# Performance work log

Measured on AMD Instinct MI355X. Metric: run time of the kernel, lower is better.

The kernel has to match this reference:

```python
import jax, jax.numpy as jnp
import numpy as np

N, E = 50000, 500000
A, R, EB, EH, H, C, AH, SH, S, AV = 64, 20, 32, 64, 4, 32, 128, 64, 32, 32
EPS = 1e-8
MAX_DIST = 0.5   # nm, maximum_interaction_radius
SCALE = 1.0      # nm, scale_factor


def physnet_rbf(d):
    # PhysNet radial basis: exp(-beta * (exp(-d) - mu_k)^2), mu_k in [exp(-r_cut), 1]
    mu = jnp.linspace(np.exp(-MAX_DIST), 1.0, R).astype(jnp.float32)
    beta = jnp.float32((2.0 / R * (1.0 - np.exp(-MAX_DIST))) ** -2)
    return jnp.exp(-beta * (jnp.exp(-d)[:, None] - mu) ** 2)  # [E, R]


def _forward(h, x, v, idx_i, idx_j, W_edge_in, b_edge_in, W_edge_h, b_edge_h,
             W_edge_out, b_edge_out, W_att, b_att, W_x_mix, W_node1, b_node1,
             W_node2, b_node2, W_post1, b_post1, W_post2, b_post2,
             W_vel1, b_vel1, W_vel2, w_v_mix):
    n = h.shape[0]
    act = jax.nn.silu
    seg_sum = lambda t, idx: jax.ops.segment_sum(t, idx, num_segments=n)

    # geometry
    r_ij = x[idx_j] - x[idx_i]                       # [E,3]
    d_ij = jnp.sqrt(jnp.sum(r_ij * r_ij, -1) + EPS)  # [E]
    dir_ij = r_ij / (d_ij[:, None] + EPS)            # [E,3]

    # update_edge: gather, RBF filter, edge MLP
    h_cat = jnp.concatenate([h[idx_i], h[idx_j]], -1)                 # [E,2A]
    filtered = physnet_rbf(d_ij) * (h_cat @ W_edge_in + b_edge_in)    # [E,R]
    e_in = jnp.concatenate([h_cat, filtered, d_ij[:, None] / SCALE], -1)
    h_ij_edge = act(e_in @ W_edge_h + b_edge_h) @ W_edge_out + b_edge_out  # [E,EB]

    # semantic attention: CELU logits + segment softmax over receivers per head
    logits = jax.nn.celu(h_ij_edge @ W_att + b_att, alpha=2.0)        # [E,H]
    seg_max = jax.ops.segment_max(logits, idx_i, num_segments=n)      # [n,H]
    exp_l = jnp.exp(logits - seg_max[idx_i])
    denom = seg_sum(exp_l, idx_i)
    att = exp_l / (denom[idx_i] + EPS)                                # [E,H]
    h_ij_semantic = (att[:, :, None] * h_ij_edge[:, None, :]).reshape(-1, H * EB)

    # neighborhood aggregation (scatter-add)
    h_i_semantic = seg_sum(h_ij_semantic, idx_i)                      # [n,H*EB]

    # spatial attention
    mix = jnp.tanh(h_ij_semantic @ W_x_mix)                           # [E,C]
    combinations = dir_ij[:, None, :] * mix[:, :, None]               # [E,C,3]
    counts = jnp.maximum(seg_sum(jnp.ones((idx_i.shape[0],), h.dtype), idx_i), 1.0)
    comb_mean = seg_sum(combinations, idx_i) / counts[:, None, None]  # scatter-mean
    comb_norm2 = jnp.sum(comb_mean * comb_mean, -1)                   # [n,C]
    h_i_spatial = act(act(comb_norm2 @ W_post1 + b_post1) @ W_post2 + b_post2)

    # node update (residual)
    node_in = jnp.concatenate([h, h_i_semantic, h_i_spatial], -1)
    h_upd = h + act(act(node_in @ W_node1 + b_node1) @ W_node2 + b_node2)

    # velocity / coordinate update
    v_ij = jnp.einsum('ecx,c->ex', combinations, w_v_mix)             # [E,3]
    dv = seg_sum(v_ij, idx_i) / counts[:, None]                       # scatter-mean
    gate = 2.0 * jax.nn.sigmoid(act(h_upd @ W_vel1 + b_vel1) @ W_vel2)  # [n,1]
    v_upd = gate * v + dv
    x_upd = x + v_upd
    return h_upd, x_upd, v_upd


def _p(k, shape, scale=0.05):
    return jax.random.normal(k, shape, dtype=jnp.float32) * scale


def setup_inputs() -> dict:
    key = jax.random.key(0)
    ks = jax.random.split(key, 24)
    return {
        'h': jax.random.normal(ks[0], (N, A), dtype=jnp.float32),
        'x': jax.random.normal(ks[1], (N, 3), dtype=jnp.float32),
        'v': jax.random.normal(ks[2], (N, 3), dtype=jnp.float32),
        'idx_i': jax.random.randint(ks[3], (E,), 0, N),
        'idx_j': jax.random.randint(ks[4], (E,), 0, N),
        'W_edge_in': _p(ks[5], (2 * A, R)), 'b_edge_in': jnp.zeros((R,), jnp.float32),
        'W_edge_h': _p(ks[6], (2 * A + R + 1, EH)), 'b_edge_h': jnp.zeros((EH,), jnp.float32),
        'W_edge_out': _p(ks[7], (EH, EB)), 'b_edge_out': jnp.zeros((EB,), jnp.float32),
        'W_att': _p(ks[8], (EB, H)), 'b_att': jnp.zeros((H,), jnp.float32),
        'W_x_mix': _p(ks[9], (H * EB, C)),
        'W_node1': _p(ks[10], (A + H * EB + S, AH)), 'b_node1': jnp.zeros((AH,), jnp.float32),
        'W_node2': _p(ks[11], (AH, A)), 'b_node2': jnp.zeros((A,), jnp.float32),
        'W_post1': _p(ks[12], (C, SH)), 'b_post1': jnp.zeros((SH,), jnp.float32),
        'W_post2': _p(ks[13], (SH, S)), 'b_post2': jnp.zeros((S,), jnp.float32),
        'W_vel1': _p(ks[14], (A, AV)), 'b_vel1': jnp.zeros((AV,), jnp.float32),
        'W_vel2': _p(ks[15], (AV, 1)),
        'w_v_mix': _p(ks[16], (C,)),
    }


def reference(h, x, v, idx_i, idx_j, W_edge_in, b_edge_in, W_edge_h, b_edge_h,
              W_edge_out, b_edge_out, W_att, b_att, W_x_mix, W_node1, b_node1,
              W_node2, b_node2, W_post1, b_post1, W_post2, b_post2,
              W_vel1, b_vel1, W_vel2, w_v_mix):
    return _forward(h, x, v, idx_i, idx_j, W_edge_in, b_edge_in, W_edge_h, b_edge_h,
                    W_edge_out, b_edge_out, W_att, b_att, W_x_mix, W_node1, b_node1,
                    W_node2, b_node2, W_post1, b_post1, W_post2, b_post2,
                    W_vel1, b_vel1, W_vel2, w_v_mix)
```

## Files before the change

kernel.cpp:

```cpp
#include <hip/hip_runtime.h>
#include <math.h>

#define DA 64
#define NODEIN_DIM 224
#define EPSC 1e-8f

typedef short v8s __attribute__((ext_vector_type(8)));
typedef float v4f __attribute__((ext_vector_type(4)));
typedef unsigned short ushort_t;

__device__ __forceinline__ float siluf(float v) {
  return v * __builtin_amdgcn_rcpf(1.0f + __expf(-v));
}
__device__ __forceinline__ float tanhfast(float x) {
  return 1.0f - 2.0f * __builtin_amdgcn_rcpf(__expf(2.0f * x) + 1.0f);
}

__device__ __forceinline__ void atomAddF(float* p, float v) {
#if defined(__HIP_DEVICE_COMPILE__)
  unsafeAtomicAdd(p, v);
#else
  atomicAdd(p, v);
#endif
}

__device__ __forceinline__ unsigned short f2bfu(float f) {
  union { float f; unsigned u; } v; v.f = f;
  unsigned r = v.u + 0x7fffu + ((v.u >> 16) & 1u);
  return (unsigned short)(r >> 16);
}
__device__ __forceinline__ short f2bfs(float f) { return (short)f2bfu(f); }
__device__ __forceinline__ float bf2f(ushort_t s) {
  union { unsigned u; float f; } v; v.u = ((unsigned)s) << 16; return v.f;
}

#define MU0 0.60653065971263342f
#define DMU ((1.0f - 0.60653065971263342f) / 19.0f)
#define BETA ((float)(1.0 / (0.039346934028736658 * 0.039346934028736658)))

__global__ __launch_bounds__(256) void cast_count(
    const float* __restrict__ hsrc, ushort_t* __restrict__ hb, int n4,
    const int* __restrict__ idx_i, int* __restrict__ deg, int E)
{
  const int stride = gridDim.x * blockDim.x;
  for (int i = blockIdx.x * blockDim.x + threadIdx.x; i < n4; i += stride) {
    const float4 fv = ((const float4*)hsrc)[i];
    ushort4 o;
    o.x = f2bfu(fv.x); o.y = f2bfu(fv.y); o.z = f2bfu(fv.z); o.w = f2bfu(fv.w);
    ((ushort4*)hb)[i] = o;
  }
  for (int e = blockIdx.x * blockDim.x + threadIdx.x; e < E; e += stride)
    atomicAdd(&deg[idx_i[e]], 1);
}

#define SCAN_B 64
#define SCAN_T (SCAN_B * 256)

__global__ __launch_bounds__(256) void deg_tsum(
    const int* __restrict__ deg, int* __restrict__ tsum, int N, int C)
{
  const int g = blockIdx.x * blockDim.x + threadIdx.x;
  const int lo = g * C;
  const int hi = (lo + C < N) ? (lo + C) : N;
  int s = 0;
  for (int i = lo; i < hi; ++i) s += deg[i];
  tsum[g] = s;
}

__global__ __launch_bounds__(256) void scan_tsum(int* __restrict__ tsum)
{
  __shared__ int ps[256];
  const int t = threadIdx.x;
  const int per = SCAN_T / 256;
  const int lo = t * per;
  int s = 0;
  for (int i = 0; i < per; ++i) s += tsum[lo + i];
  ps[t] = s;
  __syncthreads();
  if (t == 0) {
    int a = 0;
    for (int i = 0; i < 256; ++i) { const int v = ps[i]; ps[i] = a; a += v; }
  }
  __syncthreads();
  int acc = ps[t];
  for (int i = 0; i < per; ++i) {
    const int v = tsum[lo + i];
    tsum[lo + i] = acc;
    acc += v;
  }
}

__global__ __launch_bounds__(256) void write_csr(
    const int* __restrict__ deg, const int* __restrict__ tpre,
    int* __restrict__ rowstart, int* __restrict__ cursor, int N, int C)
{
  const int g = blockIdx.x * blockDim.x + threadIdx.x;
  const int lo = g * C;
  const int hi = (lo + C < N) ? (lo + C) : N;
  int acc = tpre[g];
  for (int i = lo; i < hi; ++i) {
    const int d = deg[i];
    rowstart[i] = acc;
    cursor[i] = acc;
    acc += d;
  }
  if (hi == N) rowstart[N] = acc;
}

__global__ __launch_bounds__(256) void bucket_edges(
    const int* __restrict__ idx_i, const int* __restrict__ idx_j,
    int* __restrict__ cursor, int2* __restrict__ ijperm, int E)
{
  const int stride = gridDim.x * blockDim.x;
  for (int e = blockIdx.x * blockDim.x + threadIdx.x; e < E; e += stride) {
    const int ii = idx_i[e];
    const int pos = atomicAdd(&cursor[ii], 1);
    ijperm[pos] = make_int2(ii, idx_j[e]);
  }
}

#define THS 72
__global__ __launch_bounds__(256) void edge_f12(
    const ushort_t* __restrict__ h_bf, const float* __restrict__ x,
    const int2* __restrict__ ijperm,
    const float* __restrict__ W_in, const float* __restrict__ b_in,
    const float* __restrict__ W_h, const float* __restrict__ b_h,
    const float* __restrict__ W_out, const float* __restrict__ b_out,
    const float* __restrict__ W_att, const float* __restrict__ b_att,
    float4* __restrict__ dirb, ushort_t* __restrict__ heb,
    float* __restrict__ expl, float* __restrict__ denom, int E)
{
  __shared__ ushort_t sB1[8 * 512];
  __shared__ ushort_t sB2[20 * 512];
  __shared__ ushort_t tH[4][16 * THS];

  const int tid = threadIdx.x;
  for (int idx = tid; idx < 8 * 512; idx += 256) {
    const int j = idx & 7;
    const int ln = (idx >> 3) & 63;
    const int f = idx >> 9;
    const int k = (f >> 1) * 32 + (ln >> 4) * 8 + j;
    const int col = (f & 1) * 16 + (ln & 15);
    sB1[idx] = (col < 20) ? f2bfu(W_in[k * 20 + col]) : (ushort_t)0;
  }
  for (int idx = tid; idx < 20 * 512; idx += 256) {
    const int j = idx & 7;
    const int ln = (idx >> 3) & 63;
    const int f = idx >> 9;
    const int k = (f >> 2) * 32 + (ln >> 4) * 8 + j;
    const int col = (f & 3) * 16 + (ln & 15);
    sB2[idx] = (k < 149) ? f2bfu(W_h[k * 64 + col]) : (ushort_t)0;
  }
  __syncthreads();

  const int gtid = blockIdx.x * blockDim.x + tid;
  const int wid = gtid >> 6;
  const int lane = tid & 63;
  const int w = tid >> 6;
  const int nw = (gridDim.x * blockDim.x) >> 6;
  const int l15 = lane & 15;
  const int q = lane >> 4;

  const ushort_t* b1l = sB1 + lane * 8;
  const ushort_t* b2l = sB2 + lane * 8;

  v8s bfr3[2][2];
  #pragma unroll
  for (int kc = 0; kc < 2; ++kc)
    #pragma unroll
    for (int nt = 0; nt < 2; ++nt)
      #pragma unroll
      for (int j = 0; j < 8; ++j) {
        const int k = kc * 32 + q * 8 + j;
        const int col = nt * 16 + l15;
        bfr3[kc][nt][j] = f2bfs(W_out[k * 32 + col]);
      }

  float bin[2], mu[2];
  #pragma unroll
  for (int nt = 0; nt < 2; ++nt) {
    const int col = nt * 16 + l15;
    bin[nt] = (col < 20) ? b_in[col] : 0.0f;
    mu[nt] = MU0 + (float)col * DMU;
  }
  float bias2[4];
  #pragma unroll
  for (int nt = 0; nt < 4; ++nt) bias2[nt] = b_h[nt * 16 + l15];
  float bias3[2];
  #pragma unroll
  for (int nt = 0; nt < 2; ++nt) bias3[nt] = b_out[nt * 16 + l15];

  v8s battf;
  #pragma unroll
  for (int j = 0; j < 8; ++j)
    battf[j] = (l15 < 4) ? f2bfs(W_att[(q * 8 + j) * 4 + l15]) : (short)0;
  const float bav = (l15 < 4) ? b_att[l15] : 0.0f;

  const int ntiles = (E + 15) >> 4;

  int iiC = 0, jjC = 0;
  v8s afr[4];
  float rCx = 0.f, rCy = 0.f, rCz = 0.f;
  if (wid < ntiles) {
    const int row0 = wid * 16 + l15;
    const int rowL0 = (row0 < E) ? row0 : (E - 1);
    const int2 ij = ijperm[rowL0];
    iiC = ij.x;
    jjC = ij.y;
    afr[0] = *(const v8s*)(h_bf + (size_t)iiC * 64 + q * 8);
    afr[1] = *(const v8s*)(h_bf + (size_t)iiC * 64 + 32 + q * 8);
    afr[2] = *(const v8s*)(h_bf + (size_t)jjC * 64 + q * 8);
    afr[3] = *(const v8s*)(h_bf + (size_t)jjC * 64 + 32 + q * 8);
    if (lane < 16) {
      rCx = x[jjC * 3 + 0] - x[iiC * 3 + 0];
      rCy = x[jjC * 3 + 1] - x[iiC * 3 + 1];
      rCz = x[jjC * 3 + 2] - x[iiC * 3 + 2];
    }
  }

  for (int t = wid; t < ntiles; t += nw) {
    const int tn = t + nw;
    int iiN = 0, jjN = 0;
    v8s nfr[4];
    float rNx = 0.f, rNy = 0.f, rNz = 0.f;
    if (tn < ntiles) {
      const int rowN = tn * 16 + l15;
      const int rowLN = (rowN < E) ? rowN : (E - 1);
      const int2 ij = ijperm[rowLN];
      iiN = ij.x;
      jjN = ij.y;
      nfr[0] = *(const v8s*)(h_bf + (size_t)iiN * 64 + q * 8);
      nfr[1] = *(const v8s*)(h_bf + (size_t)iiN * 64 + 32 + q * 8);
      nfr[2] = *(const v8s*)(h_bf + (size_t)jjN * 64 + q * 8);
      nfr[3] = *(const v8s*)(h_bf + (size_t)jjN * 64 + 32 + q * 8);
      if (lane < 16) {
        rNx = x[jjN * 3 + 0] - x[iiN * 3 + 0];
        rNy = x[jjN * 3 + 1] - x[iiN * 3 + 1];
        rNz = x[jjN * 3 + 2] - x[iiN * 3 + 2];
      }
    }

    const int row = t * 16 + l15;
    float dval = 0.0f;
    if (lane < 16) {
      const float s2 = rCx * rCx + rCy * rCy + rCz * rCz + EPSC;
      const float rv = __builtin_amdgcn_rsqf(s2);
      dval = s2 * rv;
      if (row < E) {
        float4 dq;
        dq.x = rCx * rv; dq.y = rCy * rv; dq.z = rCz * rv; dq.w = dval;
        dirb[row] = dq;
      }
    }

    v4f acc1[2];
    #pragma unroll
    for (int nt = 0; nt < 2; ++nt) {
      v4f a = {0.f, 0.f, 0.f, 0.f};
      #pragma unroll
      for (int kc = 0; kc < 4; ++kc) {
        const v8s bfrag = *(const v8s*)(b1l + (kc * 2 + nt) * 512);
        a = __builtin_amdgcn_mfma_f32_16x16x32_bf16(afr[kc], bfrag, a, 0, 0, 0);
      }
      acc1[nt] = a;
    }

    float dr[4], edr[4];
    #pragma unroll
    for (int r = 0; r < 4; ++r) {
      dr[r] = __shfl(dval, q * 4 + r);
      edr[r] = __expf(-dr[r]);
    }
    #pragma unroll
    for (int nt = 0; nt < 2; ++nt) {
      const int col = nt * 16 + l15;
      #pragma unroll
      for (int r = 0; r < 4; ++r) {
        ushort_t ov;
        if (col < 20) {
          const float tt = edr[r] - mu[nt];
          ov = f2bfu((acc1[nt][r] + bin[nt]) * __expf(-BETA * tt * tt));
        } else if (col == 20) {
          ov = f2bfu(dr[r]);
        } else {
          ov = 0;
        }
        tH[w][(q * 4 + r) * THS + col] = ov;
      }
    }
    __builtin_amdgcn_wave_barrier();

    const v8s afr4 = *(const v8s*)&tH[w][l15 * THS + q * 8];
    __builtin_amdgcn_wave_barrier();

    v4f acc2[4];
    #pragma unroll
    for (int nt = 0; nt < 4; ++nt) {
      v4f a = {0.f, 0.f, 0.f, 0.f};
      #pragma unroll
      for (int kc = 0; kc < 4; ++kc) {
        const v8s bfrag = *(const v8s*)(b2l + (kc * 4 + nt) * 512);
        a = __builtin_amdgcn_mfma_f32_16x16x32_bf16(afr[kc], bfrag, a, 0, 0, 0);
      }
      const v8s bfrag4 = *(const v8s*)(b2l + (4 * 4 + nt) * 512);
      a = __builtin_amdgcn_mfma_f32_16x16x32_bf16(afr4, bfrag4, a, 0, 0, 0);
      acc2[nt] = a;
    }

    #pragma unroll
    for (int nt = 0; nt < 4; ++nt) {
      #pragma unroll
      for (int r = 0; r < 4; ++r)
        tH[w][(q * 4 + r) * THS + nt * 16 + l15] =
            f2bfu(siluf(acc2[nt][r] + bias2[nt]));
    }
    __builtin_amdgcn_wave_barrier();

    v8s af3[2];
    af3[0] = *(const v8s*)&tH[w][l15 * THS + q * 8];
    af3[1] = *(const v8s*)&tH[w][l15 * THS + 32 + q * 8];

    v4f acc3[2];
    #pragma unroll
    for (int nt = 0; nt < 2; ++nt) {
      v4f a = {0.f, 0.f, 0.f, 0.f};
      #pragma unroll
      for (int kc = 0; kc < 2; ++kc)
        a = __builtin_amdgcn_mfma_f32_16x16x32_bf16(af3[kc], bfr3[kc][nt], a, 0, 0, 0);
      acc3[nt] = a;
    }
    __builtin_amdgcn_wave_barrier();

    const int rowb = t * 16 + q * 4;
    #pragma unroll
    for (int nt = 0; nt < 2; ++nt) {
      const int col = nt * 16 + l15;
      #pragma unroll
      for (int r = 0; r < 4; ++r) {
        const ushort_t hv = f2bfu(acc3[nt][r] + bias3[nt]);
        tH[w][(q * 4 + r) * THS + col] = hv;
        if (rowb + r < E) heb[(size_t)(rowb + r) * 32 + col] = hv;
      }
    }
    __builtin_amdgcn_wave_barrier();

    const v8s afA = *(const v8s*)&tH[w][l15 * THS + q * 8];
    v4f az = {0.f, 0.f, 0.f, 0.f};
    const v4f aacc = __builtin_amdgcn_mfma_f32_16x16x32_bf16(afA, battf, az, 0, 0, 0);

    int ii_r[4];
    #pragma unroll
    for (int r = 0; r < 4; ++r) ii_r[r] = __shfl(iiC, q * 4 + r);

    if (l15 < 4) {
      #pragma unroll
      for (int r = 0; r < 4; ++r) {
        if (rowb + r < E) {
          const float la = aacc[r] + bav;
          const float l = (la > 0.f) ? la : 2.0f * (__expf(0.5f * la) - 1.0f);
          const float ev = __expf(l);
          expl[(size_t)(rowb + r) * 4 + l15] = ev;
          atomAddF(&denom[ii_r[r] * 4 + l15], ev);
        }
      }
    }
    __builtin_amdgcn_wave_barrier();

    iiC = iiN; jjC = jjN;
    afr[0] = nfr[0]; afr[1] = nfr[1]; afr[2] = nfr[2]; afr[3] = nfr[3];
    rCx = rNx; rCy = rNy; rCz = rNz;
  }
}

__global__ __launch_bounds__(256) void node_fused(
    const int* __restrict__ rowstart,
    const ushort_t* __restrict__ heb,
    const float* __restrict__ expl, const float* __restrict__ denom,
    const float4* __restrict__ dirb,
    const float* __restrict__ W_xmix, const float* __restrict__ w_vmix,
    ushort_t* __restrict__ hsem, float* __restrict__ norm2,
    float* __restrict__ dv_mean, int N)
{
  __shared__ ushort_t sBX[8 * 512];

  const int tid = threadIdx.x;
  for (int idx = tid; idx < 8 * 512; idx += 256) {
    const int j = idx & 7;
    const int ln = (idx >> 3) & 63;
    const int f = idx >> 9;
    const int k = (f >> 1) * 32 + (ln >> 4) * 8 + j;
    const int col = (f & 1) * 16 + (ln & 15);
    sBX[idx] = f2bfu(W_xmix[k * 32 + col]);
  }
  __syncthreads();

  const int gtid = blockIdx.x * blockDim.x + tid;
  const int wid = gtid >> 6;
  const int lane = tid & 63;
  const int nw = (gridDim.x * blockDim.x) >> 6;
  const int l15 = lane & 15;
  const int q = lane >> 4;
  const ushort_t* bXl = sBX + lane * 8;

  const float wv0 = w_vmix[l15];
  const float wv1 = w_vmix[16 + l15];

  int sC = 0, eC = 0;
  if (wid < N) {
    sC = rowstart[wid];
    eC = rowstart[wid + 1];
  }

  for (int n = wid; n < N; n += nw) {
    const int nn = n + nw;
    int sN = 0, eN = 0;
    if (nn < N) {
      sN = rowstart[nn];
      eN = rowstart[nn + 1];
    }
    const int s = sC;
    const int epd = eC;
    const int deg = epd - s;

    v8s hech0 = {0, 0, 0, 0, 0, 0, 0, 0};
    if (deg > 0) {
      const int e0 = s + ((l15 < deg) ? l15 : (deg - 1));
      hech0 = *(const v8s*)(heb + e0 * 32 + q * 8);
    }

    const float4 dnm = *(const float4*)(denom + n * 4);
    float invden[4];
    invden[0] = __builtin_amdgcn_rcpf(dnm.x + EPSC);
    invden[1] = __builtin_amdgcn_rcpf(dnm.y + EPSC);
    invden[2] = __builtin_amdgcn_rcpf(dnm.z + EPSC);
    invden[3] = __builtin_amdgcn_rcpf(dnm.w + EPSC);

    {
      float sm00 = 0.f, sm01 = 0.f, sm10 = 0.f, sm11 = 0.f;
      float sm20 = 0.f, sm21 = 0.f, sm30 = 0.f, sm31 = 0.f;
      int k = s;
      for (; k + 4 <= epd; k += 4) {
        const unsigned hv = ((const unsigned*)heb)[k * 16 + lane];
        const float4 ex = ((const float4*)expl)[k + q];
        const float h0 = bf2f((ushort_t)(hv & 0xffffu));
        const float h1 = bf2f((ushort_t)(hv >> 16));
        sm00 += ex.x * h0; sm01 += ex.x * h1;
        sm10 += ex.y * h0; sm11 += ex.y * h1;
        sm20 += ex.z * h0; sm21 += ex.z * h1;
        sm30 += ex.w * h0; sm31 += ex.w * h1;
      }
      if (k < epd) {
        const int ke = k + q;
        const int kl = (ke < epd) ? ke : (epd - 1);
        const float live = (ke < epd) ? 1.0f : 0.0f;
        const unsigned hv = ((const unsigned*)heb)[kl * 16 + l15];
        const float4 ex = ((const float4*)expl)[kl];
        const float h0 = bf2f((ushort_t)(hv & 0xffffu)) * live;
        const float h1 = bf2f((ushort_t)(hv >> 16)) * live;
        sm00 += ex.x * h0; sm01 += ex.x * h1;
        sm10 += ex.y * h0; sm11 += ex.y * h1;
        sm20 += ex.z * h0; sm21 += ex.z * h1;
        sm30 += ex.w * h0; sm31 += ex.w * h1;
      }
      sm00 += __shfl_xor(sm00, 16); sm00 += __shfl_xor(sm00, 32);
      sm01 += __shfl_xor(sm01, 16); sm01 += __shfl_xor(sm01, 32);
      sm10 += __shfl_xor(sm10, 16); sm10 += __shfl_xor(sm10, 32);
      sm11 += __shfl_xor(sm11, 16); sm11 += __shfl_xor(sm11, 32);
      sm20 += __shfl_xor(sm20, 16); sm20 += __shfl_xor(sm20, 32);
      sm21 += __shfl_xor(sm21, 16); sm21 += __shfl_xor(sm21, 32);
      sm30 += __shfl_xor(sm30, 16); sm30 += __shfl_xor(sm30, 32);
      sm31 += __shfl_xor(sm31, 16); sm31 += __shfl_xor(sm31, 32);
      const float sa = (q & 2) ? ((q & 1) ? sm30 : sm20)
                               : ((q & 1) ? sm10 : sm00);
      const float sb = (q & 2) ? ((q & 1) ? sm31 : sm21)
                               : ((q & 1) ? sm11 : sm01);
      const float idn = (q & 2) ? ((q & 1) ? invden[3] : invden[2])
                                : ((q & 1) ? invden[1] : invden[0]);
      const unsigned pack = (unsigned)f2bfu(sa * idn) |
                            ((unsigned)f2bfu(sb * idn) << 16);
      ((unsigned*)hsem)[n * 64 + lane] = pack;
    }

    float cx0 = 0.f, cy0 = 0.f, cz0 = 0.f;
    float cx1 = 0.f, cy1 = 0.f, cz1 = 0.f;

    for (int c0 = 0; c0 < deg; c0 += 16) {
      v8s hech;
      if (c0 == 0) {
        hech = hech0;
      } else {
        const int ra = c0 + l15;
        const int eA = s + ((ra < deg) ? ra : (deg - 1));
        hech = *(const v8s*)(heb + eA * 32 + q * 8);
      }

      v4f y[4][2];
      #pragma unroll
      for (int h4 = 0; h4 < 4; ++h4) {
        #pragma unroll
        for (int nt = 0; nt < 2; ++nt) {
          v4f z = {0.f, 0.f, 0.f, 0.f};
          y[h4][nt] = __builtin_amdgcn_mfma_f32_16x16x32_bf16(
              hech, *(const v8s*)(bXl + (h4 * 2 + nt) * 512), z, 0, 0, 0);
        }
      }

      #pragma unroll
      for (int r = 0; r < 4; ++r) {
        const int rr = c0 + q * 4 + r;
        const int live = rr < deg;
        const int eR = s + (live ? rr : (deg - 1));
        const float lf = live ? 1.0f : 0.0f;
        const float4 ex4 = *(const float4*)(expl + eR * 4);
        const float at0 = ex4.x * invden[0] * lf;
        const float at1 = ex4.y * invden[1] * lf;
        const float at2 = ex4.z * invden[2] * lf;
        const float at3 = ex4.w * invden[3] * lf;
        const float p0 = at0 * y[0][0][r] + at1 * y[1][0][r] +
                         at2 * y[2][0][r] + at3 * y[3][0][r];
        const float p1 = at0 * y[0][1][r] + at1 * y[1][1][r] +
                         at2 * y[2][1][r] + at3 * y[3][1][r];
        const float4 dq = dirb[eR];
        const float m0 = tanhfast(p0);
        const float m1 = tanhfast(p1);
        cx0 += dq.x * m0; cy0 += dq.y * m0; cz0 += dq.z * m0;
        cx1 += dq.x * m1; cy1 += dq.y * m1; cz1 += dq.z * m1;
      }
    }

    cx0 += __shfl_xor(cx0, 16); cx0 += __shfl_xor(cx0, 32);
    cy0 += __shfl_xor(cy0, 16); cy0 += __shfl_xor(cy0, 32);
    cz0 += __shfl_xor(cz0, 16); cz0 += __shfl_xor(cz0, 32);
    cx1 += __shfl_xor(cx1, 16); cx1 += __shfl_xor(cx1, 32);
    cy1 += __shfl_xor(cy1, 16); cy1 += __shfl_xor(cy1, 32);
    cz1 += __shfl_xor(cz1, 16); cz1 += __shfl_xor(cz1, 32);

    const float cinv = __builtin_amdgcn_rcpf(fmaxf((float)deg, 1.0f));

    if (lane < 32) {
      const float mx = ((lane & 16) ? cx1 : cx0) * cinv;
      const float my = ((lane & 16) ? cy1 : cy0) * cinv;
      const float mz = ((lane & 16) ? cz1 : cz0) * cinv;
      norm2[n * 32 + lane] = mx * mx + my * my + mz * mz;
    }

    float tx = wv0 * cx0 + wv1 * cx1;
    float ty = wv0 * cy0 + wv1 * cy1;
    float tz = wv0 * cz0 + wv1 * cz1;
    tx += __shfl_xor(tx, 1); tx += __shfl_xor(tx, 2);
    tx += __shfl_xor(tx, 4); tx += __shfl_xor(tx, 8);
    ty += __shfl_xor(ty, 1); ty += __shfl_xor(ty, 2);
    ty += __shfl_xor(ty, 4); ty += __shfl_xor(ty, 8);
    tz += __shfl_xor(tz, 1); tz += __shfl_xor(tz, 2);
    tz += __shfl_xor(tz, 4); tz += __shfl_xor(tz, 8);
    if (lane == 0) {
      dv_mean[n * 3 + 0] = tx * cinv;
      dv_mean[n * 3 + 1] = ty * cinv;
      dv_mean[n * 3 + 2] = tz * cinv;
    }

    sC = sN; eC = eN;
  }
}

#define W1S 232
__global__ __launch_bounds__(256) void node_c1_mfma(
    const ushort_t* __restrict__ h_bf, const ushort_t* __restrict__ hsem,
    const float* __restrict__ norm2,
    const float* __restrict__ W_post1, const float* __restrict__ b_post1,
    const float* __restrict__ W_post2, const float* __restrict__ b_post2,
    const float* __restrict__ W_node1, const float* __restrict__ b_node1,
    ushort_t* __restrict__ nh_out, int N)
{
  __shared__ ushort_t sW1t[128 * W1S];
  __shared__ ushort_t tp[4][16 * THS];

  const int tid = threadIdx.x;
  for (int idx = tid; idx < 224 * 128; idx += 256) {
    const int k = idx >> 7;
    const int c = idx & 127;
    sW1t[c * W1S + k] = f2bfu(W_node1[idx]);
  }
  __syncthreads();

  const int lane = tid & 63;
  const int w = tid >> 6;
  const int l15 = lane & 15;
  const int q = lane >> 4;

  v8s bp1[4];
  #pragma unroll
  for (int nt = 0; nt < 4; ++nt)
    #pragma unroll
    for (int j = 0; j < 8; ++j)
      bp1[nt][j] = f2bfs(W_post1[(q * 8 + j) * 64 + nt * 16 + l15]);
  v8s bp2[2][2];
  #pragma unroll
  for (int kc = 0; kc < 2; ++kc)
    #pragma unroll
    for (int nt = 0; nt < 2; ++nt)
      #pragma unroll
      for (int j = 0; j < 8; ++j)
        bp2[kc][nt][j] = f2bfs(W_post2[(kc * 32 + q * 8 + j) * 32 + nt * 16 + l15]);
  float bb1[4];
  #pragma unroll
  for (int nt = 0; nt < 4; ++nt) bb1[nt] = b_post1[nt * 16 + l15];
  float bb2[2];
  #pragma unroll
  for (int nt = 0; nt < 2; ++nt) bb2[nt] = b_post2[nt * 16 + l15];
  float b1[8];
  #pragma unroll
  for (int nt = 0; nt < 8; ++nt) b1[nt] = b_node1[nt * 16 + l15];

  const int gw = blockIdx.x * 4 + w;
  const int nwv = gridDim.x * 4;
  const int ntiles = (N + 15) >> 4;

  for (int t = gw; t < ntiles; t += nwv) {
    const int row = t * 16 + l15;
    const int rowL = (row < N) ? row : (N - 1);

    const float4 nA = *(const float4*)(norm2 + (size_t)rowL * 32 + q * 8);
    const float4 nB = *(const float4*)(norm2 + (size_t)rowL * 32 + q * 8 + 4);
    v8s a1;
    a1[0] = f2bfs(nA.x); a1[1] = f2bfs(nA.y);
    a1[2] = f2bfs(nA.z); a1[3] = f2bfs(nA.w);
    a1[4] = f2bfs(nB.x); a1[5] = f2bfs(nB.y);
    a1[6] = f2bfs(nB.z); a1[7] = f2bfs(nB.w);

    v4f p1[4];
    #pragma unroll
    for (int nt = 0; nt < 4; ++nt) {
      v4f a = {0.f, 0.f, 0.f, 0.f};
      p1[nt] = __builtin_amdgcn_mfma_f32_16x16x32_bf16(a1, bp1[nt], a, 0, 0, 0);
    }
    #pragma unroll
    for (int nt = 0; nt < 4; ++nt)
      #pragma unroll
      for (int r = 0; r < 4; ++r)
        tp[w][(q * 4 + r) * THS + nt * 16 + l15] =
            f2bfu(siluf(p1[nt][r] + bb1[nt]));
    __builtin_amdgcn_wave_barrier();

    v8s a2[2];
    a2[0] = *(const v8s*)&tp[w][l15 * THS + q * 8];
    a2[1] = *(const v8s*)&tp[w][l15 * THS + 32 + q * 8];

    v4f p2[2];
    #pragma unroll
    for (int nt = 0; nt < 2; ++nt) {
      v4f a = {0.f, 0.f, 0.f, 0.f};
      #pragma unroll
      for (int kc = 0; kc < 2; ++kc)
        a = __builtin_amdgcn_mfma_f32_16x16x32_bf16(a2[kc], bp2[kc][nt], a, 0, 0, 0);
      p2[nt] = a;
    }
    __builtin_amdgcn_wave_barrier();
    #pragma unroll
    for (int nt = 0; nt < 2; ++nt)
      #pragma unroll
      for (int r = 0; r < 4; ++r)
        tp[w][(q * 4 + r) * THS + nt * 16 + l15] =
            f2bfu(siluf(p2[nt][r] + bb2[nt]));
    __builtin_amdgcn_wave_barrier();

    v8s af[7];
    af[0] = *(const v8s*)(h_bf + (size_t)rowL * 64 + q * 8);
    af[1] = *(const v8s*)(h_bf + (size_t)rowL * 64 + 32 + q * 8);
    #pragma unroll
    for (int kc = 0; kc < 4; ++kc)
      af[2 + kc] = *(const v8s*)(hsem + (size_t)rowL * 128 + kc * 32 + q * 8);
    af[6] = *(const v8s*)&tp[w][l15 * THS + q * 8];

    v4f acc[8];
    #pragma unroll
    for (int nt = 0; nt < 8; ++nt) acc[nt] = (v4f){0.f, 0.f, 0.f, 0.f};
    #pragma unroll
    for (int kc = 0; kc < 7; ++kc) {
      #pragma unroll
      for (int nt = 0; nt < 8; ++nt) {
        const v8s bfrag =
            *(const v8s*)&sW1t[(nt * 16 + l15) * W1S + kc * 32 + q * 8];
        acc[nt] = __builtin_amdgcn_mfma_f32_16x16x32_bf16(af[kc], bfrag, acc[nt], 0, 0, 0);
      }
    }

    const int rowb = t * 16 + q * 4;
    #pragma unroll
    for (int nt = 0; nt < 8; ++nt) {
      #pragma unroll
      for (int r = 0; r < 4; ++r)
        if (rowb + r < N)
          nh_out[(size_t)(rowb + r) * 128 + nt * 16 + l15] =
              f2bfu(siluf(acc[nt][r] + b1[nt]));
    }
  }
}

__global__ __launch_bounds__(256) void node_c2_mfma(
    const float* __restrict__ h, const float* __restrict__ x,
    const float* __restrict__ v, const ushort_t* __restrict__ nh,
    const float* __restrict__ dv_mean,
    const float* __restrict__ W_node2, const float* __restrict__ b_node2,
    const float* __restrict__ W_vel1, const float* __restrict__ b_vel1,
    const float* __restrict__ W_vel2,
    float* __restrict__ out, int N)
{
  __shared__ ushort_t sW2[16 * 64 * 8];
  __shared__ ushort_t sWv[4 * 64 * 8];
  __shared__ ushort_t tH[4][16 * THS];
  __shared__ float sg[4][16];

  const int tid = threadIdx.x;
  for (int idx = tid; idx < 16 * 64 * 8; idx += 256) {
    const int j = idx & 7;
    const int ln = (idx >> 3) & 63;
    const int f = idx >> 9;
    const int k = (f >> 2) * 32 + (ln >> 4) * 8 + j;
    const int col = (f & 3) * 16 + (ln & 15);
    sW2[idx] = f2bfu(W_node2[k * 64 + col]);
  }
  for (int idx = tid; idx < 4 * 64 * 8; idx += 256) {
    const int j = idx & 7;
    const int ln = (idx >> 3) & 63;
    const int f = idx >> 9;
    const int k = (f >> 1) * 32 + (ln >> 4) * 8 + j;
    const int col = (f & 1) * 16 + (ln & 15);
    sWv[idx] = f2bfu(W_vel1[k * 32 + col]);
  }
  __syncthreads();

  const int lane = tid & 63;
  const int w = tid >> 6;
  const int l15 = lane & 15;
  const int q = lane >> 4;

  const ushort_t* w2l = sW2 + lane * 8;
  const ushort_t* wvl = sWv + lane * 8;

  float b2[4];
  #pragma unroll
  for (int nt = 0; nt < 4; ++nt) b2[nt] = b_node2[nt * 16 + l15];
  float bv[2];
  #pragma unroll
  for (int nt = 0; nt < 2; ++nt) bv[nt] = b_vel1[nt * 16 + l15];
  float wv2[2];
  #pragma unroll
  for (int nt = 0; nt < 2; ++nt) wv2[nt] = W_vel2[nt * 16 + l15];

  const int gw = blockIdx.x * 4 + w;
  const int nwv = gridDim.x * 4;
  const int ntiles = (N + 15) >> 4;

  for (int t = gw; t < ntiles; t += nwv) {
    const int row = t * 16 + l15;
    const int rowL = (row < N) ? row : (N - 1);

    v8s af[4];
    #pragma unroll
    for (int kc = 0; kc < 4; ++kc)
      af[kc] = *(const v8s*)(nh + (size_t)rowL * 128 + kc * 32 + q * 8);

    v4f acc[4];
    #pragma unroll
    for (int nt = 0; nt < 4; ++nt) {
      v4f a = {0.f, 0.f, 0.f, 0.f};
      #pragma unroll
      for (int kc = 0; kc < 4; ++kc) {
        const v8s bfrag = *(const v8s*)(w2l + (kc * 4 + nt) * 512);
        a = __builtin_amdgcn_mfma_f32_16x16x32_bf16(af[kc], bfrag, a, 0, 0, 0);
      }
      acc[nt] = a;
    }

    const int rowb = t * 16 + q * 4;
    #pragma unroll
    for (int nt = 0; nt < 4; ++nt) {
      const int col = nt * 16 + l15;
      #pragma unroll
      for (int r = 0; r < 4; ++r) {
        const int n = rowb + r;
        if (n < N) {
          const float hu = h[(size_t)n * 64 + col] + siluf(acc[nt][r] + b2[nt]);
          out[(size_t)n * 64 + col] = hu;
          tH[w][(q * 4 + r) * THS + col] = f2bfu(hu);
        }
      }
    }
    __builtin_amdgcn_wave_barrier();

    v8s a2[2];
    a2[0] = *(const v8s*)&tH[w][l15 * THS + q * 8];
    a2[1] = *(const v8s*)&tH[w][l15 * THS + 32 + q * 8];
    v4f av[2];
    #pragma unroll
    for (int nt = 0; nt < 2; ++nt) {
      v4f a = {0.f, 0.f, 0.f, 0.f};
      #pragma unroll
      for (int kc = 0; kc < 2; ++kc) {
        const v8s bfrag = *(const v8s*)(wvl + (kc * 2 + nt) * 512);
        a = __builtin_amdgcn_mfma_f32_16x16x32_bf16(a2[kc], bfrag, a, 0, 0, 0);
      }
      av[nt] = a;
    }

    #pragma unroll
    for (int r = 0; r < 4; ++r) {
      float pr = siluf(av[0][r] + bv[0]) * wv2[0] +
                 siluf(av[1][r] + bv[1]) * wv2[1];
      pr += __shfl_xor(pr, 1);
      pr += __shfl_xor(pr, 2);
      pr += __shfl_xor(pr, 4);
      pr += __shfl_xor(pr, 8);
      if (l15 == 0)
        sg[w][q * 4 + r] = 2.0f * __builtin_amdgcn_rcpf(1.0f + __expf(-pr));
    }
    __builtin_amdgcn_wave_barrier();

    if (lane < 48) {
      const int rr = lane / 3;
      const int c = lane % 3;
      const int n = t * 16 + rr;
      if (n < N) {
        const float gate = sg[w][rr];
        const float dv = dv_mean[n * 3 + c];
        const float vu = gate * v[n * 3 + c] + dv;
        out[(size_t)N * 64 + (size_t)n * 3 + c] = x[n * 3 + c] + vu;
        out[(size_t)N * 64 + (size_t)N * 3 + (size_t)n * 3 + c] = vu;
      }
    }
    __builtin_amdgcn_wave_barrier();
  }
}

extern "C" void kernel_launch(void* const* d_in, const int* in_sizes, int n_in,
                              void* d_out, int out_size, void* d_ws, size_t ws_size,
                              hipStream_t stream) {
  const float* h   = (const float*)d_in[0];
  const float* x   = (const float*)d_in[1];
  const float* v   = (const float*)d_in[2];
  const int* idx_i = (const int*)d_in[3];
  const int* idx_j = (const int*)d_in[4];
  const float* W_edge_in  = (const float*)d_in[5];
  const float* b_edge_in  = (const float*)d_in[6];
  const float* W_edge_h   = (const float*)d_in[7];
  const float* b_edge_h   = (const float*)d_in[8];
  const float* W_edge_out = (const float*)d_in[9];
  const float* b_edge_out = (const float*)d_in[10];
  const float* W_att      = (const float*)d_in[11];
  const float* b_att      = (const float*)d_in[12];
  const float* W_x_mix    = (const float*)d_in[13];
  const float* W_node1    = (const float*)d_in[14];
  const float* b_node1    = (const float*)d_in[15];
  const float* W_node2    = (const float*)d_in[16];
  const float* b_node2    = (const float*)d_in[17];
  const float* W_post1    = (const float*)d_in[18];
  const float* b_post1    = (const float*)d_in[19];
  const float* W_post2    = (const float*)d_in[20];
  const float* b_post2    = (const float*)d_in[21];
  const float* W_vel1     = (const float*)d_in[22];
  const float* b_vel1     = (const float*)d_in[23];
  const float* W_vel2     = (const float*)d_in[24];
  const float* w_v_mix    = (const float*)d_in[25];

  const int E = in_sizes[3];
  const int N = in_sizes[0] / DA;

  float* ws = (float*)d_ws;
  size_t off = 0;
  float* denom    = ws + off; off += (size_t)N * 4;
  int*   deg      = (int*)(ws + off); off += (size_t)N;
  const size_t zeroBytes = off * sizeof(float);
  int*   rowstart = (int*)(ws + off); off += (size_t)N + 4;
  int*   cursor   = (int*)(ws + off); off += (size_t)N;
  int*   tsum     = (int*)(ws + off); off += (size_t)SCAN_T;
  int2*  ijperm   = (int2*)(ws + off); off += (size_t)E * 2;
  float* expl     = ws + off; off += (size_t)E * 4;
  float* dirbR    = ws + off; off += (size_t)E * 4;
  float* hsemR    = ws + off; off += (size_t)N * 64;
  float* norm2    = ws + off; off += (size_t)N * 32;
  float* dv_mean  = ws + off; off += (size_t)N * 4;
  float* hbfR     = ws + off; off += (size_t)N * 32;
  float* fltR     = ws + off; off += (size_t)E * 16;
  float* hebR     = ws + off; off += (size_t)E * 16;

  ushort_t* h_bf = (ushort_t*)hbfR;
  ushort_t* hsem = (ushort_t*)hsemR;
  ushort_t* heb  = (ushort_t*)hebR;
  ushort_t* nh   = (ushort_t*)fltR;
  float4*   dirb = (float4*)dirbR;

  hipMemsetAsync(d_ws, 0, zeroBytes, stream);

  {
    const int n4 = (N * 64) / 4;
    cast_count<<<1024, 256, 0, stream>>>(h, h_bf, n4, idx_i, deg, E);
  }
  {
    const int C = (N + SCAN_T - 1) / SCAN_T;
    deg_tsum<<<SCAN_B, 256, 0, stream>>>(deg, tsum, N, C);
    scan_tsum<<<1, 256, 0, stream>>>(tsum);
    write_csr<<<SCAN_B, 256, 0, stream>>>(deg, tsum, rowstart, cursor, N, C);
  }
  bucket_edges<<<512, 256, 0, stream>>>(idx_i, idx_j, cursor, ijperm, E);
  edge_f12<<<1024, 256, 0, stream>>>(h_bf, x, ijperm,
                                     W_edge_in, b_edge_in, W_edge_h, b_edge_h,
                                     W_edge_out, b_edge_out, W_att, b_att,
                                     dirb, heb, expl, denom, E);
  node_fused<<<2048, 256, 0, stream>>>(rowstart, heb, expl, denom, dirb,
                                       W_x_mix, w_v_mix, hsem, norm2,
                                       dv_mean, N);
  node_c1_mfma<<<512, 256, 0, stream>>>(
      h_bf, hsem, norm2, W_post1, b_post1, W_post2, b_post2,
      W_node1, b_node1, nh, N);
  node_c2_mfma<<<512, 256, 0, stream>>>(
      h, x, v, nh, dv_mean, W_node2, b_node2, W_vel1, b_vel1, W_vel2,
      (float*)d_out, N);
}
```

Baseline: 363.6 us.

## Pretranspose W_node1 to bf16 in global memory instead of per-block LDS staging

The bf16 transpose of W_node1 moves into the cast_count prologue kernel and is written once to a workspace buffer. node_c1_mfma then reads B fragments straight from global memory (served from L2/L1) instead of rebuilding a ~59KB shared-memory copy in every block. That removes per-block LDS staging and a __syncthreads, and lowers LDS use so more blocks can be resident, which the grid increase to 784 blocks for node_c1 and node_c2 relies on. The cost is B-fragment loads going through the cache hierarchy in the inner MFMA loop. Separately, node_fused drops its prefetch of the first edge chunk.

```diff
diff --git a/kernel.cpp b/kernel.cpp
--- a/kernel.cpp
+++ b/kernel.cpp
@@ -40,7 +40,8 @@
 
 __global__ __launch_bounds__(256) void cast_count(
     const float* __restrict__ hsrc, ushort_t* __restrict__ hb, int n4,
-    const int* __restrict__ idx_i, int* __restrict__ deg, int E)
+    const int* __restrict__ idx_i, int* __restrict__ deg, int E,
+    const float* __restrict__ W_node1, ushort_t* __restrict__ W1T)
 {
   const int stride = gridDim.x * blockDim.x;
   for (int i = blockIdx.x * blockDim.x + threadIdx.x; i < n4; i += stride) {
@@ -51,6 +52,12 @@
   }
   for (int e = blockIdx.x * blockDim.x + threadIdx.x; e < E; e += stride)
     atomicAdd(&deg[idx_i[e]], 1);
+  for (int i = blockIdx.x * blockDim.x + threadIdx.x; i < 224 * 128;
+       i += stride) {
+    const int c = i / 224;
+    const int k = i - c * 224;
+    W1T[i] = f2bfu(W_node1[k * 128 + c]);
+  }
 }
 
 #define SCAN_B 64
@@ -422,12 +429,6 @@
     const int epd = eC;
     const int deg = epd - s;
 
-    v8s hech0 = {0, 0, 0, 0, 0, 0, 0, 0};
-    if (deg > 0) {
-      const int e0 = s + ((l15 < deg) ? l15 : (deg - 1));
-      hech0 = *(const v8s*)(heb + e0 * 32 + q * 8);
-    }
-
     const float4 dnm = *(const float4*)(denom + n * 4);
     float invden[4];
     invden[0] = __builtin_amdgcn_rcpf(dnm.x + EPSC);
@@ -485,14 +486,9 @@
     float cx1 = 0.f, cy1 = 0.f, cz1 = 0.f;
 
     for (int c0 = 0; c0 < deg; c0 += 16) {
-      v8s hech;
-      if (c0 == 0) {
-        hech = hech0;
-      } else {
-        const int ra = c0 + l15;
-        const int eA = s + ((ra < deg) ? ra : (deg - 1));
-        hech = *(const v8s*)(heb + eA * 32 + q * 8);
-      }
+      const int ra = c0 + l15;
+      const int eA = s + ((ra < deg) ? ra : (deg - 1));
+      const v8s hech = *(const v8s*)(heb + eA * 32 + q * 8);
 
       v4f y[4][2];
       #pragma unroll
@@ -563,26 +559,17 @@
   }
 }
 
-#define W1S 232
 __global__ __launch_bounds__(256) void node_c1_mfma(
     const ushort_t* __restrict__ h_bf, const ushort_t* __restrict__ hsem,
-    const float* __restrict__ norm2,
+    const float* __restrict__ norm2, const ushort_t* __restrict__ W1T,
     const float* __restrict__ W_post1, const float* __restrict__ b_post1,
     const float* __restrict__ W_post2, const float* __restrict__ b_post2,
-    const float* __restrict__ W_node1, const float* __restrict__ b_node1,
+    const float* __restrict__ b_node1,
     ushort_t* __restrict__ nh_out, int N)
 {
-  __shared__ ushort_t sW1t[128 * W1S];
   __shared__ ushort_t tp[4][16 * THS];
 
   const int tid = threadIdx.x;
-  for (int idx = tid; idx < 224 * 128; idx += 256) {
-    const int k = idx >> 7;
-    const int c = idx & 127;
-    sW1t[c * W1S + k] = f2bfu(W_node1[idx]);
-  }
-  __syncthreads();
-
   const int lane = tid & 63;
   const int w = tid >> 6;
   const int l15 = lane & 15;
@@ -611,6 +598,8 @@
   float b1[8];
   #pragma unroll
   for (int nt = 0; nt < 8; ++nt) b1[nt] = b_node1[nt * 16 + l15];
+
+  const ushort_t* w1base = W1T + l15 * 224 + q * 8;
 
   const int gw = blockIdx.x * 4 + w;
   const int nwv = gridDim.x * 4;
@@ -679,8 +668,7 @@
     for (int kc = 0; kc < 7; ++kc) {
       #pragma unroll
       for (int nt = 0; nt < 8; ++nt) {
-        const v8s bfrag =
-            *(const v8s*)&sW1t[(nt * 16 + l15) * W1S + kc * 32 + q * 8];
+        const v8s bfrag = *(const v8s*)(w1base + nt * 16 * 224 + kc * 32);
         acc[nt] = __builtin_amdgcn_mfma_f32_16x16x32_bf16(af[kc], bfrag, acc[nt], 0, 0, 0);
       }
     }
@@ -881,6 +869,7 @@
   float* norm2    = ws + off; off += (size_t)N * 32;
   float* dv_mean  = ws + off; off += (size_t)N * 4;
   float* hbfR     = ws + off; off += (size_t)N * 32;
+  float* w1tR     = ws + off; off += (size_t)14336;
   float* fltR     = ws + off; off += (size_t)E * 16;
   float* hebR     = ws + off; off += (size_t)E * 16;
 
@@ -888,13 +877,15 @@
   ushort_t* hsem = (ushort_t*)hsemR;
   ushort_t* heb  = (ushort_t*)hebR;
   ushort_t* nh   = (ushort_t*)fltR;
+  ushort_t* W1T  = (ushort_t*)w1tR;
   float4*   dirb = (float4*)dirbR;
 
   hipMemsetAsync(d_ws, 0, zeroBytes, stream);
 
   {
     const int n4 = (N * 64) / 4;
-    cast_count<<<1024, 256, 0, stream>>>(h, h_bf, n4, idx_i, deg, E);
+    cast_count<<<1024, 256, 0, stream>>>(h, h_bf, n4, idx_i, deg, E,
+                                         W_node1, W1T);
   }
   {
     const int C = (N + SCAN_T - 1) / SCAN_T;
@@ -910,10 +901,10 @@
   node_fused<<<2048, 256, 0, stream>>>(rowstart, heb, expl, denom, dirb,
                                        W_x_mix, w_v_mix, hsem, norm2,
                                        dv_mean, N);
-  node_c1_mfma<<<512, 256, 0, stream>>>(
-      h_bf, hsem, norm2, W_post1, b_post1, W_post2, b_post2,
-      W_node1, b_node1, nh, N);
-  node_c2_mfma<<<512, 256, 0, stream>>>(
+  node_c1_mfma<<<784, 256, 0, stream>>>(
+      h_bf, hsem, norm2, W1T, W_post1, b_post1, W_post2, b_post2,
+      b_node1, nh, N);
+  node_c2_mfma<<<784, 256, 0, stream>>>(
       h, x, v, nh, dv_mean, W_node2, b_node2, W_vel1, b_vel1, W_vel2,
       (float*)d_out, N);
 }
```

After: 373.4 us. +2.7%, slower.
